# Optimization experiments

Hardware: AMD Instinct MI355X
Metric: run time of the kernel (lower is better)

Reference implementation:

```python
import jax, jax.numpy as jnp
import numpy as np

B, A, N_IN = 128, 96, 128  # molecules, atoms per molecule, feature dim
H1, H2 = 64, 1             # gated-equivariant MLP widths: 128 -> 64 -> 1


def _mlp(x, W1, b1, W2, b2):
    return jax.nn.silu(x @ W1 + b1) @ W2 + b2


def _gated_block(s, v, Wmix, Ws1, bs1, Ws2, bs2, n_out, sact):
    # s: [N, n_sin], v: [N, 3, n_vin]
    vmix = jnp.einsum('ndi,io->ndo', v, Wmix)          # [N, 3, 2*n_out]
    vV, vW = vmix[..., :n_out], vmix[..., n_out:]
    vVn = jnp.linalg.norm(vV, axis=-2)                 # [N, n_out]
    x = _mlp(jnp.concatenate([s, vVn], axis=-1), Ws1, bs1, Ws2, bs2)
    s_out, gate = x[..., :n_out], x[..., n_out:]
    v_out = gate[:, None, :] * vW                      # [N, 3, n_out]
    if sact:
        s_out = jax.nn.silu(s_out)
    return s_out, v_out


def setup_inputs():
    key = jax.random.key(0)
    ks = iter(jax.random.split(key, 40))
    def W(shape):
        return jax.random.normal(next(ks), shape, jnp.float32) / np.sqrt(shape[0]).astype(np.float32)
    N = B * A
    return dict(
        positions=jax.random.normal(next(ks), (N, 3), jnp.float32) * 3.0,
        scalar_rep=jax.random.normal(next(ks), (N, N_IN), jnp.float32),
        vector_rep=jax.random.normal(next(ks), (N, 3, N_IN), jnp.float32),
        mix_W1=W((N_IN, 2 * H1)),
        sc1_W1=W((N_IN + H1, N_IN)), sc1_b1=jnp.zeros((N_IN,), jnp.float32),
        sc1_W2=W((N_IN, 2 * H1)), sc1_b2=jnp.zeros((2 * H1,), jnp.float32),
        mix_W2=W((H1, 2 * H2)),
        sc2_W1=W((H1 + H2, H1)), sc2_b1=jnp.zeros((H1,), jnp.float32),
        sc2_W2=W((H1, 2 * H2)), sc2_b2=jnp.zeros((2 * H2,), jnp.float32),
        vv_W1=W((9, 30)), vv_b1=jnp.zeros((30,), jnp.float32), vv_W2=W((30, 9)), vv_b2=jnp.zeros((9,), jnp.float32),
        vr_W1=W((9, 30)), vr_b1=jnp.zeros((30,), jnp.float32), vr_W2=W((30, 9)), vr_b2=jnp.zeros((9,), jnp.float32),
        s_W1=W((2, 30)), s_b1=jnp.zeros((30,), jnp.float32), s_W2=W((30, 9)), s_b2=jnp.zeros((9,), jnp.float32),
        h_W1=W((9, 30)), h_b1=jnp.zeros((30,), jnp.float32), h_W2=W((30, 9)), h_b2=jnp.zeros((9,), jnp.float32),
        n_atoms=jnp.full((B,), A, dtype=jnp.int32),
    )


def reference(positions, scalar_rep, vector_rep,
              mix_W1, sc1_W1, sc1_b1, sc1_W2, sc1_b2,
              mix_W2, sc2_W1, sc2_b1, sc2_W2, sc2_b2,
              vv_W1, vv_b1, vv_W2, vv_b2,
              vr_W1, vr_b1, vr_W2, vr_b2,
              s_W1, s_b1, s_W2, s_b2,
              h_W1, h_b1, h_W2, h_b2, n_atoms):
    # outnet: gated equivariant MLP 128 -> 64 (silu on scalars) -> 1 (no sact)
    s, v = _gated_block(scalar_rep, vector_rep, mix_W1, sc1_W1, sc1_b1, sc1_W2, sc1_b2, H1, True)
    s, v = _gated_block(s, v, mix_W2, sc2_W1, sc2_b1, sc2_W2, sc2_b2, H2, False)
    l0 = s[:, 0].reshape(B, A)          # [B, A]
    l1 = v[:, :, 0].reshape(B, A, 3)    # [B, A, 3]
    pos = positions.reshape(B, A, 3)
    # per-pair outer products, flattened 3x3 -> 9 (row-major k,l as in torch view)
    vv = jnp.einsum('bik,bjl->bijkl', l1, l1).reshape(B, A, A, 9)
    vr = jnp.einsum('bik,bjl->bijkl', l1, pos).reshape(B, A, A, 9)
    vv = _mlp(vv, vv_W1, vv_b1, vv_W2, vv_b2)
    vr = _mlp(vr, vr_W1, vr_b1, vr_W2, vr_b2)
    sp = jnp.stack([jnp.broadcast_to(l0[:, :, None], (B, A, A)),
                    jnp.broadcast_to(l0[:, None, :], (B, A, A))], axis=-1)  # [B,A,A,2] = (s_i, s_j)
    sp = _mlp(sp, s_W1, s_b1, s_W2, s_b2)
    h = _mlp(vv + vr + sp, h_W1, h_b1, h_W2, h_b2).reshape(B, A, A, 3, 3)
    # permute(0,2,1,3) per molecule -> block Hessian [3A, 3A]
    h = jnp.transpose(h, (0, 1, 3, 2, 4)).reshape(B, 3 * A, 3 * A)
    return h.reshape(-1, 27)
```

## Files before the change

### kernel.cpp

```cpp
#include <hip/hip_runtime.h>
#include <cstddef>

#define A_ATOMS 96
#define BATCH   128
#define NNODES  12288
#define NB      8
#define AS      132
#define XS      196

typedef float v2f __attribute__((ext_vector_type(2)));

__device__ __forceinline__ float silu_f(float x) {
    float e = __expf(-x);
    return x * __builtin_amdgcn_rcpf(1.0f + e);
}
__device__ __forceinline__ v2f silu2(v2f x) {
    v2f r; r.x = silu_f(x.x); r.y = silu_f(x.y); return r;
}

#define RED64(v) { v += __shfl_xor(v, 1); v += __shfl_xor(v, 2); v += __shfl_xor(v, 4); \
                   v += __shfl_xor(v, 8); v += __shfl_xor(v, 16); v += __shfl_xor(v, 32); }
#define RED8(v)  { v += __shfl_xor(v, 1); v += __shfl_xor(v, 2); v += __shfl_xor(v, 4); }

__global__ __launch_bounds__(256)
void node_k(const float* __restrict__ vrep, const float* __restrict__ mixW1,
            const float* __restrict__ srep,
            const float* __restrict__ sc1W1, const float* __restrict__ sc1b1,
            const float* __restrict__ sc1W2, const float* __restrict__ sc1b2,
            const float* __restrict__ mixW2,
            const float* __restrict__ sc2W1, const float* __restrict__ sc2b1,
            const float* __restrict__ sc2W2, const float* __restrict__ sc2b2,
            float* __restrict__ l0v, float* __restrict__ l1v) {
    __shared__ float AsL[24 * AS];
    __shared__ float xinS[NB * XS];
    __shared__ float s1s[4][64];
    __shared__ float pwp[NB][2][6];

    const int t  = threadIdx.x;
    const int w  = t >> 6;
    const int ln = t & 63;
    const int cx = ln & 7;
    const int ry = ln >> 3;
    const int cb = w * 32 + cx * 4;
    const int row0  = blockIdx.x * 24;
    const int node0 = blockIdx.x * NB;

#pragma unroll
    for (int it = 0; it < 3; it++) {
        const int idx = it * 256 + t;
        const int r   = idx >> 5;
        const int c4  = (idx & 31) * 4;
        *(float4*)&AsL[r * AS + c4] = *(const float4*)(vrep + (size_t)(row0 + r) * 128 + c4);
    }
    {
        const int a  = t >> 5;
        const int c4 = (t & 31) * 4;
        *(float4*)&xinS[a * XS + c4] = *(const float4*)(srep + (size_t)(node0 + a) * 128 + c4);
    }
    __syncthreads();

    float acc[3][4];
#pragma unroll
    for (int i = 0; i < 3; i++)
#pragma unroll
        for (int j = 0; j < 4; j++) acc[i][j] = 0.0f;

    for (int kc = 0; kc < 128; kc += 8) {
        float a0[8], a1[8], a2[8];
        *(float4*)&a0[0] = *(const float4*)&AsL[(3 * ry + 0) * AS + kc];
        *(float4*)&a0[4] = *(const float4*)&AsL[(3 * ry + 0) * AS + kc + 4];
        *(float4*)&a1[0] = *(const float4*)&AsL[(3 * ry + 1) * AS + kc];
        *(float4*)&a1[4] = *(const float4*)&AsL[(3 * ry + 1) * AS + kc + 4];
        *(float4*)&a2[0] = *(const float4*)&AsL[(3 * ry + 2) * AS + kc];
        *(float4*)&a2[4] = *(const float4*)&AsL[(3 * ry + 2) * AS + kc + 4];
#pragma unroll
        for (int kk = 0; kk < 8; kk++) {
            float b[4];
            *(float4*)b = *(const float4*)(mixW1 + (size_t)(kc + kk) * 128 + cb);
#pragma unroll
            for (int j = 0; j < 4; j++) {
                acc[0][j] += a0[kk] * b[j];
                acc[1][j] += a1[kk] * b[j];
                acc[2][j] += a2[kk] * b[j];
            }
        }
    }
    if (w < 2) {
        float nrm[4];
#pragma unroll
        for (int c = 0; c < 4; c++)
            nrm[c] = sqrtf(acc[0][c] * acc[0][c] + acc[1][c] * acc[1][c]
                         + acc[2][c] * acc[2][c]);
        *(float4*)&xinS[ry * XS + 128 + cb] = *(float4*)nrm;
    }
    __syncthreads();

    float* workS = AsL;
    {
        float acc3[4];
#pragma unroll
        for (int j = 0; j < 4; j++) acc3[j] = 0.0f;
        for (int kc = 0; kc < 192; kc += 8) {
            float af[8];
            *(float4*)&af[0] = *(const float4*)&xinS[ry * XS + kc];
            *(float4*)&af[4] = *(const float4*)&xinS[ry * XS + kc + 4];
#pragma unroll
            for (int kk = 0; kk < 8; kk++) {
                float b[4];
                *(float4*)b = *(const float4*)(sc1W1 + (size_t)(kc + kk) * 128 + cb);
#pragma unroll
                for (int j = 0; j < 4; j++) acc3[j] += af[kk] * b[j];
            }
        }
        float h[4];
#pragma unroll
        for (int j = 0; j < 4; j++) h[j] = silu_f(acc3[j] + sc1b1[cb + j]);
        __syncthreads();
        *(float4*)&workS[ry * AS + cb] = *(float4*)h;
    }
    __syncthreads();

    float xg[4];
    {
        float acc4[4];
#pragma unroll
        for (int j = 0; j < 4; j++) acc4[j] = 0.0f;
        for (int kc = 0; kc < 128; kc += 8) {
            float af[8];
            *(float4*)&af[0] = *(const float4*)&workS[ry * AS + kc];
            *(float4*)&af[4] = *(const float4*)&workS[ry * AS + kc + 4];
#pragma unroll
            for (int kk = 0; kk < 8; kk++) {
                float b[4];
                *(float4*)b = *(const float4*)(sc1W2 + (size_t)(kc + kk) * 128 + cb);
#pragma unroll
                for (int j = 0; j < 4; j++) acc4[j] += af[kk] * b[j];
            }
        }
        if (w < 2) {
            float xs[4];
#pragma unroll
            for (int j = 0; j < 4; j++) xs[j] = acc4[j] + sc1b2[cb + j];
            *(float4*)&xinS[ry * XS + cb] = *(float4*)xs;
        } else {
#pragma unroll
            for (int j = 0; j < 4; j++) xg[j] = acc4[j] + sc1b2[cb + j];
        }
    }

    if (w >= 2) {
        float p0 = 0, p1 = 0, p2 = 0, p3 = 0, p4 = 0, p5 = 0;
#pragma unroll
        for (int c = 0; c < 4; c++) {
            float2 m = *(const float2*)(mixW2 + (size_t)(cb - 64 + c) * 2);
            const float v0 = xg[c] * acc[0][c];
            const float v1 = xg[c] * acc[1][c];
            const float v2 = xg[c] * acc[2][c];
            p0 += v0 * m.x; p1 += v0 * m.y;
            p2 += v1 * m.x; p3 += v1 * m.y;
            p4 += v2 * m.x; p5 += v2 * m.y;
        }
        RED8(p0); RED8(p1); RED8(p2); RED8(p3); RED8(p4); RED8(p5);
        if (cx == 0) {
            pwp[ry][w - 2][0] = p0; pwp[ry][w - 2][1] = p1;
            pwp[ry][w - 2][2] = p2; pwp[ry][w - 2][3] = p3;
            pwp[ry][w - 2][4] = p4; pwp[ry][w - 2][5] = p5;
        }
    }
    __syncthreads();

    {
        const float bb1 = sc2b1[ln];
        const float wn  = sc2W1[64 * 64 + ln];
        const float wq0 = sc2W2[ln * 2 + 0], wq1 = sc2W2[ln * 2 + 1];
#pragma unroll
        for (int r = 0; r < 2; r++) {
            const int nl = r * 4 + w;
            const float q00 = pwp[nl][0][0] + pwp[nl][1][0];
            const float q01 = pwp[nl][0][1] + pwp[nl][1][1];
            const float q10 = pwp[nl][0][2] + pwp[nl][1][2];
            const float q11 = pwp[nl][0][3] + pwp[nl][1][3];
            const float q20 = pwp[nl][0][4] + pwp[nl][1][4];
            const float q21 = pwp[nl][0][5] + pwp[nl][1][5];
            const float vn2 = sqrtf(q00 * q00 + q10 * q10 + q20 * q20);
            const float s1 = silu_f(xinS[nl * XS + ln]);
            s1s[w][ln] = s1;
            __builtin_amdgcn_s_waitcnt(0);
            float acc5 = bb1 + vn2 * wn;
#pragma unroll 8
            for (int i2 = 0; i2 < 64; i2++) acc5 += s1s[w][i2] * sc2W1[i2 * 64 + ln];
            const float h2 = silu_f(acc5);
            float q0 = h2 * wq0, q1 = h2 * wq1;
            RED64(q0); RED64(q1);
            if (ln == 0) {
                const int n = node0 + nl;
                const float gate = q1 + sc2b2[1];
                l0v[n] = q0 + sc2b2[0];
                l1v[(size_t)n * 3 + 0] = gate * q01;
                l1v[(size_t)n * 3 + 1] = gate * q11;
                l1v[(size_t)n * 3 + 2] = gate * q21;
            }
        }
    }
}

__global__ __launch_bounds__(256)
void pairpre_k(const float* __restrict__ l1v, const float* __restrict__ pos,
               const float* __restrict__ l0v,
               const float* __restrict__ vvW1, const float* __restrict__ vrW1,
               const float* __restrict__ sW1, const float* __restrict__ sb1,
               float* __restrict__ Pv, float* __restrict__ Pr,
               float* __restrict__ Ps) {
    const int jl = threadIdx.x & 31;
    const int hq = threadIdx.x >> 5;
    const int j  = blockIdx.x * 32 + jl;
    const float lj0 = l1v[j * 3 + 0], lj1 = l1v[j * 3 + 1], lj2 = l1v[j * 3 + 2];
    const float pj0 = pos[j * 3 + 0], pj1 = pos[j * 3 + 1], pj2 = pos[j * 3 + 2];
    const float l0j = l0v[j];
#pragma unroll
    for (int hh = 0; hh < 4; hh++) {
        const int h = hq * 4 + hh;
        if (h < 30) {
#pragma unroll
            for (int a = 0; a < 3; a++) {
                float v = lj0 * vvW1[(3 * a + 0) * 30 + h] + lj1 * vvW1[(3 * a + 1) * 30 + h]
                        + lj2 * vvW1[(3 * a + 2) * 30 + h];
                float r = pj0 * vrW1[(3 * a + 0) * 30 + h] + pj1 * vrW1[(3 * a + 1) * 30 + h]
                        + pj2 * vrW1[(3 * a + 2) * 30 + h];
                Pv[(size_t)(a * 30 + h) * NNODES + j] = v;
                Pr[(size_t)(a * 30 + h) * NNODES + j] = r;
            }
            Ps[(size_t)h * NNODES + j] = sb1[h] + l0j * sW1[30 + h];
        }
    }
}

__global__ __launch_bounds__(192)
void pair_k(const float* __restrict__ l0v, const float* __restrict__ l1v,
            const float* __restrict__ Pv, const float* __restrict__ Pr,
            const float* __restrict__ Ps,
            const float* __restrict__ vvb1, const float* __restrict__ vrb1,
            const float* __restrict__ sW1,
            const float* __restrict__ vvW2, const float* __restrict__ vrW2,
            const float* __restrict__ sW2,
            const float* __restrict__ vvb2, const float* __restrict__ vrb2,
            const float* __restrict__ sb2,
            const float* __restrict__ hW1,  const float* __restrict__ hb1,
            const float* __restrict__ hW2,  const float* __restrict__ hb2,
            float* __restrict__ out) {
    const int t = threadIdx.x;
    const int b = blockIdx.y;
    const int g = (t >= 96) ? 1 : 0;
    const int j = t - g * 96;
    const int i0 = blockIdx.x * 4 + g * 2;
    const int ni0 = b * A_ATOMS + i0;
    const int ni1 = ni0 + 1;
    const int nj  = b * A_ATOMS + j;

    const v2f li0 = { l1v[ni0 * 3 + 0], l1v[ni1 * 3 + 0] };
    const v2f li1 = { l1v[ni0 * 3 + 1], l1v[ni1 * 3 + 1] };
    const v2f li2 = { l1v[ni0 * 3 + 2], l1v[ni1 * 3 + 2] };
    const v2f s0i = { l0v[ni0], l0v[ni1] };

    v2f t9[9];
#pragma unroll
    for (int l = 0; l < 9; l++) t9[l] = (v2f)(vvb2[l] + vrb2[l] + sb2[l]);

    for (int h = 0; h < 30; h++) {
        const float pv0 = Pv[(size_t)h * NNODES + nj];
        const float pv1 = Pv[(size_t)(30 + h) * NNODES + nj];
        const float pv2 = Pv[(size_t)(60 + h) * NNODES + nj];
        const float pr0 = Pr[(size_t)h * NNODES + nj];
        const float pr1 = Pr[(size_t)(30 + h) * NNODES + nj];
        const float pr2 = Pr[(size_t)(60 + h) * NNODES + nj];
        const float ps  = Ps[(size_t)h * NNODES + nj];

        v2f av = (v2f)(vvb1[h]) + li0 * pv0 + li1 * pv1 + li2 * pv2;
        v2f ar = (v2f)(vrb1[h]) + li0 * pr0 + li1 * pr1 + li2 * pr2;
        v2f as = (v2f)(ps) + s0i * sW1[h];
        av = silu2(av); ar = silu2(ar); as = silu2(as);
#pragma unroll
        for (int l = 0; l < 9; l++)
            t9[l] += av * vvW2[h * 9 + l] + ar * vrW2[h * 9 + l] + as * sW2[h * 9 + l];
    }

    v2f o9[9];
#pragma unroll
    for (int l = 0; l < 9; l++) o9[l] = (v2f)(hb2[l]);
    for (int h = 0; h < 30; h++) {
        v2f a = (v2f)(hb1[h]);
#pragma unroll
        for (int m = 0; m < 9; m++) a += t9[m] * hW1[m * 30 + h];
        a = silu2(a);
#pragma unroll
        for (int l = 0; l < 9; l++) o9[l] += a * hW2[h * 9 + l];
    }

    const size_t rb0 = (size_t)ni0;
#pragma unroll
    for (int k = 0; k < 3; k++) {
        const size_t off0 = (rb0 * 3 + k) * 288 + (size_t)j * 3;
        const size_t off1 = off0 + 3 * 288;
        out[off0 + 0] = o9[3 * k + 0].x;
        out[off0 + 1] = o9[3 * k + 1].x;
        out[off0 + 2] = o9[3 * k + 2].x;
        out[off1 + 0] = o9[3 * k + 0].y;
        out[off1 + 1] = o9[3 * k + 1].y;
        out[off1 + 2] = o9[3 * k + 2].y;
    }
}

extern "C" void kernel_launch(void* const* d_in, const int* in_sizes, int n_in,
                              void* d_out, int out_size, void* d_ws, size_t ws_size,
                              hipStream_t stream) {
    const float* pos   = (const float*)d_in[0];
    const float* srep  = (const float*)d_in[1];
    const float* vrep  = (const float*)d_in[2];
    const float* mixW1 = (const float*)d_in[3];
    const float* sc1W1 = (const float*)d_in[4];
    const float* sc1b1 = (const float*)d_in[5];
    const float* sc1W2 = (const float*)d_in[6];
    const float* sc1b2 = (const float*)d_in[7];
    const float* mixW2 = (const float*)d_in[8];
    const float* sc2W1 = (const float*)d_in[9];
    const float* sc2b1 = (const float*)d_in[10];
    const float* sc2W2 = (const float*)d_in[11];
    const float* sc2b2 = (const float*)d_in[12];
    const float* vvW1  = (const float*)d_in[13];
    const float* vvb1  = (const float*)d_in[14];
    const float* vvW2  = (const float*)d_in[15];
    const float* vvb2  = (const float*)d_in[16];
    const float* vrW1  = (const float*)d_in[17];
    const float* vrb1  = (const float*)d_in[18];
    const float* vrW2  = (const float*)d_in[19];
    const float* vrb2  = (const float*)d_in[20];
    const float* sW1   = (const float*)d_in[21];
    const float* sb1   = (const float*)d_in[22];
    const float* sW2   = (const float*)d_in[23];
    const float* sb2   = (const float*)d_in[24];
    const float* hW1   = (const float*)d_in[25];
    const float* hb1   = (const float*)d_in[26];
    const float* hW2   = (const float*)d_in[27];
    const float* hb2   = (const float*)d_in[28];

    float* ws  = (float*)d_ws;
    float* Pv  = ws;
    float* Pr  = Pv + 1105920;
    float* Ps  = Pr + 1105920;
    float* l0v = Ps + 368640;
    float* l1v = l0v + 12288;
    float* outf = (float*)d_out;

    node_k<<<NNODES / NB, 256, 0, stream>>>(
        vrep, mixW1, srep,
        sc1W1, sc1b1, sc1W2, sc1b2,
        mixW2, sc2W1, sc2b1, sc2W2, sc2b2,
        l0v, l1v);

    pairpre_k<<<NNODES / 32, 256, 0, stream>>>(l1v, pos, l0v, vvW1, vrW1,
                                               sW1, sb1, Pv, Pr, Ps);

    pair_k<<<dim3(A_ATOMS / 4, BATCH), 192, 0, stream>>>(
        l0v, l1v, Pv, Pr, Ps,
        vvb1, vrb1, sW1,
        vvW2, vrW2, sW2,
        vvb2, vrb2, sb2,
        hW1, hb1, hW2, hb2,
        outf);
}
```

Before: 292.7 us.

## Halve node kernel block size and compute two node rows per thread

The node kernel drops from 256 to 128 threads per block. Each thread now accumulates two node rows (p=0,1) across 64-column slices, so every weight float4 loaded from global memory feeds twice as many FMAs. The second-layer gated MLP processes four nodes per wavefront with a shared weight load per input index instead of looping node by node. The cost is higher register pressure per thread (launch bounds 128,3) and fewer waves per block to hide latency.

```diff
diff --git a/kernel.cpp b/kernel.cpp
--- a/kernel.cpp
+++ b/kernel.cpp
@@ -20,9 +20,10 @@
 
 #define RED64(v) { v += __shfl_xor(v, 1); v += __shfl_xor(v, 2); v += __shfl_xor(v, 4); \
                    v += __shfl_xor(v, 8); v += __shfl_xor(v, 16); v += __shfl_xor(v, 32); }
-#define RED8(v)  { v += __shfl_xor(v, 1); v += __shfl_xor(v, 2); v += __shfl_xor(v, 4); }
-
-__global__ __launch_bounds__(256)
+#define RED16(v) { v += __shfl_xor(v, 1); v += __shfl_xor(v, 2); v += __shfl_xor(v, 4); \
+                   v += __shfl_xor(v, 8); }
+
+__global__ __launch_bounds__(128, 3)
 void node_k(const float* __restrict__ vrep, const float* __restrict__ mixW1,
             const float* __restrict__ srep,
             const float* __restrict__ sc1W1, const float* __restrict__ sc1b1,
@@ -33,138 +34,175 @@
             float* __restrict__ l0v, float* __restrict__ l1v) {
     __shared__ float AsL[24 * AS];
     __shared__ float xinS[NB * XS];
-    __shared__ float s1s[4][64];
-    __shared__ float pwp[NB][2][6];
+    __shared__ float s1s[2][4][64];
+    __shared__ float pwp[NB][6];
 
     const int t  = threadIdx.x;
     const int w  = t >> 6;
     const int ln = t & 63;
-    const int cx = ln & 7;
-    const int ry = ln >> 3;
-    const int cb = w * 32 + cx * 4;
+    const int cx = ln & 15;
+    const int ry = ln >> 4;
+    const int cb = w * 64 + cx * 4;
     const int row0  = blockIdx.x * 24;
     const int node0 = blockIdx.x * NB;
 
 #pragma unroll
-    for (int it = 0; it < 3; it++) {
-        const int idx = it * 256 + t;
+    for (int it = 0; it < 6; it++) {
+        const int idx = it * 128 + t;
         const int r   = idx >> 5;
         const int c4  = (idx & 31) * 4;
         *(float4*)&AsL[r * AS + c4] = *(const float4*)(vrep + (size_t)(row0 + r) * 128 + c4);
     }
-    {
-        const int a  = t >> 5;
-        const int c4 = (t & 31) * 4;
+#pragma unroll
+    for (int it = 0; it < 2; it++) {
+        const int idx = it * 128 + t;
+        const int a   = idx >> 5;
+        const int c4  = (idx & 31) * 4;
         *(float4*)&xinS[a * XS + c4] = *(const float4*)(srep + (size_t)(node0 + a) * 128 + c4);
     }
     __syncthreads();
 
-    float acc[3][4];
-#pragma unroll
-    for (int i = 0; i < 3; i++)
-#pragma unroll
-        for (int j = 0; j < 4; j++) acc[i][j] = 0.0f;
+    float acc[2][3][4];
+#pragma unroll
+    for (int p = 0; p < 2; p++)
+#pragma unroll
+        for (int d = 0; d < 3; d++)
+#pragma unroll
+            for (int j = 0; j < 4; j++) acc[p][d][j] = 0.0f;
 
     for (int kc = 0; kc < 128; kc += 8) {
-        float a0[8], a1[8], a2[8];
-        *(float4*)&a0[0] = *(const float4*)&AsL[(3 * ry + 0) * AS + kc];
-        *(float4*)&a0[4] = *(const float4*)&AsL[(3 * ry + 0) * AS + kc + 4];
-        *(float4*)&a1[0] = *(const float4*)&AsL[(3 * ry + 1) * AS + kc];
-        *(float4*)&a1[4] = *(const float4*)&AsL[(3 * ry + 1) * AS + kc + 4];
-        *(float4*)&a2[0] = *(const float4*)&AsL[(3 * ry + 2) * AS + kc];
-        *(float4*)&a2[4] = *(const float4*)&AsL[(3 * ry + 2) * AS + kc + 4];
+        float a[2][3][8];
+#pragma unroll
+        for (int p = 0; p < 2; p++)
+#pragma unroll
+            for (int d = 0; d < 3; d++) {
+                const int row = (3 * (ry + 4 * p) + d) * AS + kc;
+                *(float4*)&a[p][d][0] = *(const float4*)&AsL[row];
+                *(float4*)&a[p][d][4] = *(const float4*)&AsL[row + 4];
+            }
 #pragma unroll
         for (int kk = 0; kk < 8; kk++) {
             float b[4];
             *(float4*)b = *(const float4*)(mixW1 + (size_t)(kc + kk) * 128 + cb);
 #pragma unroll
-            for (int j = 0; j < 4; j++) {
-                acc[0][j] += a0[kk] * b[j];
-                acc[1][j] += a1[kk] * b[j];
-                acc[2][j] += a2[kk] * b[j];
-            }
-        }
-    }
-    if (w < 2) {
-        float nrm[4];
-#pragma unroll
-        for (int c = 0; c < 4; c++)
-            nrm[c] = sqrtf(acc[0][c] * acc[0][c] + acc[1][c] * acc[1][c]
-                         + acc[2][c] * acc[2][c]);
-        *(float4*)&xinS[ry * XS + 128 + cb] = *(float4*)nrm;
+            for (int p = 0; p < 2; p++)
+#pragma unroll
+                for (int d = 0; d < 3; d++)
+#pragma unroll
+                    for (int j = 0; j < 4; j++)
+                        acc[p][d][j] += a[p][d][kk] * b[j];
+        }
+    }
+    if (w == 0) {
+#pragma unroll
+        for (int p = 0; p < 2; p++) {
+            float nrm[4];
+#pragma unroll
+            for (int c = 0; c < 4; c++)
+                nrm[c] = sqrtf(acc[p][0][c] * acc[p][0][c] + acc[p][1][c] * acc[p][1][c]
+                             + acc[p][2][c] * acc[p][2][c]);
+            *(float4*)&xinS[(ry + 4 * p) * XS + 128 + cb] = *(float4*)nrm;
+        }
     }
     __syncthreads();
 
     float* workS = AsL;
     {
-        float acc3[4];
-#pragma unroll
-        for (int j = 0; j < 4; j++) acc3[j] = 0.0f;
+        float acc3[2][4];
+#pragma unroll
+        for (int p = 0; p < 2; p++)
+#pragma unroll
+            for (int j = 0; j < 4; j++) acc3[p][j] = 0.0f;
         for (int kc = 0; kc < 192; kc += 8) {
-            float af[8];
-            *(float4*)&af[0] = *(const float4*)&xinS[ry * XS + kc];
-            *(float4*)&af[4] = *(const float4*)&xinS[ry * XS + kc + 4];
+            float af[2][8];
+#pragma unroll
+            for (int p = 0; p < 2; p++) {
+                const int row = (ry + 4 * p) * XS + kc;
+                *(float4*)&af[p][0] = *(const float4*)&xinS[row];
+                *(float4*)&af[p][4] = *(const float4*)&xinS[row + 4];
+            }
 #pragma unroll
             for (int kk = 0; kk < 8; kk++) {
                 float b[4];
                 *(float4*)b = *(const float4*)(sc1W1 + (size_t)(kc + kk) * 128 + cb);
 #pragma unroll
-                for (int j = 0; j < 4; j++) acc3[j] += af[kk] * b[j];
-            }
-        }
-        float h[4];
-#pragma unroll
-        for (int j = 0; j < 4; j++) h[j] = silu_f(acc3[j] + sc1b1[cb + j]);
-        __syncthreads();
-        *(float4*)&workS[ry * AS + cb] = *(float4*)h;
+                for (int p = 0; p < 2; p++)
+#pragma unroll
+                    for (int j = 0; j < 4; j++) acc3[p][j] += af[p][kk] * b[j];
+            }
+        }
+#pragma unroll
+        for (int p = 0; p < 2; p++) {
+            float h[4];
+#pragma unroll
+            for (int j = 0; j < 4; j++) h[j] = silu_f(acc3[p][j] + sc1b1[cb + j]);
+            *(float4*)&workS[(ry + 4 * p) * AS + cb] = *(float4*)h;
+        }
     }
     __syncthreads();
 
-    float xg[4];
+    float xg[2][4];
     {
-        float acc4[4];
-#pragma unroll
-        for (int j = 0; j < 4; j++) acc4[j] = 0.0f;
+        float acc4[2][4];
+#pragma unroll
+        for (int p = 0; p < 2; p++)
+#pragma unroll
+            for (int j = 0; j < 4; j++) acc4[p][j] = 0.0f;
         for (int kc = 0; kc < 128; kc += 8) {
-            float af[8];
-            *(float4*)&af[0] = *(const float4*)&workS[ry * AS + kc];
-            *(float4*)&af[4] = *(const float4*)&workS[ry * AS + kc + 4];
+            float af[2][8];
+#pragma unroll
+            for (int p = 0; p < 2; p++) {
+                const int row = (ry + 4 * p) * AS + kc;
+                *(float4*)&af[p][0] = *(const float4*)&workS[row];
+                *(float4*)&af[p][4] = *(const float4*)&workS[row + 4];
+            }
 #pragma unroll
             for (int kk = 0; kk < 8; kk++) {
                 float b[4];
                 *(float4*)b = *(const float4*)(sc1W2 + (size_t)(kc + kk) * 128 + cb);
 #pragma unroll
-                for (int j = 0; j < 4; j++) acc4[j] += af[kk] * b[j];
-            }
-        }
-        if (w < 2) {
-            float xs[4];
-#pragma unroll
-            for (int j = 0; j < 4; j++) xs[j] = acc4[j] + sc1b2[cb + j];
-            *(float4*)&xinS[ry * XS + cb] = *(float4*)xs;
+                for (int p = 0; p < 2; p++)
+#pragma unroll
+                    for (int j = 0; j < 4; j++) acc4[p][j] += af[p][kk] * b[j];
+            }
+        }
+        if (w == 0) {
+#pragma unroll
+            for (int p = 0; p < 2; p++) {
+                float xs[4];
+#pragma unroll
+                for (int j = 0; j < 4; j++) xs[j] = acc4[p][j] + sc1b2[cb + j];
+                *(float4*)&xinS[(ry + 4 * p) * XS + cb] = *(float4*)xs;
+            }
         } else {
 #pragma unroll
-            for (int j = 0; j < 4; j++) xg[j] = acc4[j] + sc1b2[cb + j];
-        }
-    }
-
-    if (w >= 2) {
-        float p0 = 0, p1 = 0, p2 = 0, p3 = 0, p4 = 0, p5 = 0;
-#pragma unroll
-        for (int c = 0; c < 4; c++) {
-            float2 m = *(const float2*)(mixW2 + (size_t)(cb - 64 + c) * 2);
-            const float v0 = xg[c] * acc[0][c];
-            const float v1 = xg[c] * acc[1][c];
-            const float v2 = xg[c] * acc[2][c];
-            p0 += v0 * m.x; p1 += v0 * m.y;
-            p2 += v1 * m.x; p3 += v1 * m.y;
-            p4 += v2 * m.x; p5 += v2 * m.y;
-        }
-        RED8(p0); RED8(p1); RED8(p2); RED8(p3); RED8(p4); RED8(p5);
-        if (cx == 0) {
-            pwp[ry][w - 2][0] = p0; pwp[ry][w - 2][1] = p1;
-            pwp[ry][w - 2][2] = p2; pwp[ry][w - 2][3] = p3;
-            pwp[ry][w - 2][4] = p4; pwp[ry][w - 2][5] = p5;
+            for (int p = 0; p < 2; p++)
+#pragma unroll
+                for (int j = 0; j < 4; j++) xg[p][j] = acc4[p][j] + sc1b2[cb + j];
+        }
+    }
+
+    if (w == 1) {
+#pragma unroll
+        for (int p = 0; p < 2; p++) {
+            float p0 = 0, p1 = 0, p2 = 0, p3 = 0, p4 = 0, p5 = 0;
+#pragma unroll
+            for (int c = 0; c < 4; c++) {
+                float2 m = *(const float2*)(mixW2 + (size_t)(cb - 64 + c) * 2);
+                const float v0 = xg[p][c] * acc[p][0][c];
+                const float v1 = xg[p][c] * acc[p][1][c];
+                const float v2 = xg[p][c] * acc[p][2][c];
+                p0 += v0 * m.x; p1 += v0 * m.y;
+                p2 += v1 * m.x; p3 += v1 * m.y;
+                p4 += v2 * m.x; p5 += v2 * m.y;
+            }
+            RED16(p0); RED16(p1); RED16(p2); RED16(p3); RED16(p4); RED16(p5);
+            if (cx == 0) {
+                const int nl = ry + 4 * p;
+                pwp[nl][0] = p0; pwp[nl][1] = p1;
+                pwp[nl][2] = p2; pwp[nl][3] = p3;
+                pwp[nl][4] = p4; pwp[nl][5] = p5;
+            }
         }
     }
     __syncthreads();
@@ -173,32 +211,37 @@
         const float bb1 = sc2b1[ln];
         const float wn  = sc2W1[64 * 64 + ln];
         const float wq0 = sc2W2[ln * 2 + 0], wq1 = sc2W2[ln * 2 + 1];
-#pragma unroll
-        for (int r = 0; r < 2; r++) {
-            const int nl = r * 4 + w;
-            const float q00 = pwp[nl][0][0] + pwp[nl][1][0];
-            const float q01 = pwp[nl][0][1] + pwp[nl][1][1];
-            const float q10 = pwp[nl][0][2] + pwp[nl][1][2];
-            const float q11 = pwp[nl][0][3] + pwp[nl][1][3];
-            const float q20 = pwp[nl][0][4] + pwp[nl][1][4];
-            const float q21 = pwp[nl][0][5] + pwp[nl][1][5];
-            const float vn2 = sqrtf(q00 * q00 + q10 * q10 + q20 * q20);
-            const float s1 = silu_f(xinS[nl * XS + ln]);
-            s1s[w][ln] = s1;
-            __builtin_amdgcn_s_waitcnt(0);
-            float acc5 = bb1 + vn2 * wn;
+        float vn2[4], g0[4], g1[4], g2[4];
+#pragma unroll
+        for (int r = 0; r < 4; r++) {
+            const int nl = r * 2 + w;
+            const float q00 = pwp[nl][0], q10 = pwp[nl][2], q20 = pwp[nl][4];
+            vn2[r] = sqrtf(q00 * q00 + q10 * q10 + q20 * q20);
+            g0[r] = pwp[nl][1]; g1[r] = pwp[nl][3]; g2[r] = pwp[nl][5];
+            s1s[w][r][ln] = silu_f(xinS[nl * XS + ln]);
+        }
+        __builtin_amdgcn_s_waitcnt(0);
+        float acc5[4];
+#pragma unroll
+        for (int r = 0; r < 4; r++) acc5[r] = bb1 + vn2[r] * wn;
 #pragma unroll 8
-            for (int i2 = 0; i2 < 64; i2++) acc5 += s1s[w][i2] * sc2W1[i2 * 64 + ln];
-            const float h2 = silu_f(acc5);
+        for (int i2 = 0; i2 < 64; i2++) {
+            const float wv = sc2W1[i2 * 64 + ln];
+#pragma unroll
+            for (int r = 0; r < 4; r++) acc5[r] += s1s[w][r][i2] * wv;
+        }
+#pragma unroll
+        for (int r = 0; r < 4; r++) {
+            const float h2 = silu_f(acc5[r]);
             float q0 = h2 * wq0, q1 = h2 * wq1;
             RED64(q0); RED64(q1);
             if (ln == 0) {
-                const int n = node0 + nl;
+                const int n = node0 + r * 2 + w;
                 const float gate = q1 + sc2b2[1];
                 l0v[n] = q0 + sc2b2[0];
-                l1v[(size_t)n * 3 + 0] = gate * q01;
-                l1v[(size_t)n * 3 + 1] = gate * q11;
-                l1v[(size_t)n * 3 + 2] = gate * q21;
+                l1v[(size_t)n * 3 + 0] = gate * g0[r];
+                l1v[(size_t)n * 3 + 1] = gate * g1[r];
+                l1v[(size_t)n * 3 + 2] = gate * g2[r];
             }
         }
     }
@@ -351,7 +394,7 @@
     float* l1v = l0v + 12288;
     float* outf = (float*)d_out;
 
-    node_k<<<NNODES / NB, 256, 0, stream>>>(
+    node_k<<<NNODES / NB, 128, 0, stream>>>(
         vrep, mixW1, srep,
         sc1W1, sc1b1, sc1W2, sc1b2,
         mixW2, sc2W1, sc2b1, sc2W2, sc2b2,
```

After: 261.0 us. 10.8% less time.
